# Optimization experiments

Hardware: AMD Instinct MI355X
Metric: run time of the kernel (lower is better)

## Reference

```python
import jax, jax.numpy as jnp
import numpy as np

N = 50000          # num_nodes
E = 800000         # num_edges (avg degree 16)
HID = 128          # hidden_dim
NH = 8             # num_heads
HD = 16            # head_dim
FFN = 512          # ffn_dim
EPS = 1e-5


def setup_inputs() -> dict:
    key = jax.random.key(0)
    ks = jax.random.split(key, 12)
    s = 0.02
    d = {}
    d["x"] = jax.random.normal(ks[0], (N, HID), jnp.float32)
    d["edge_index"] = jax.random.randint(ks[1], (2, E), 0, N, dtype=jnp.int32)
    # projection weights stored as [in, out] (math identical to torch Linear)
    d["Wq"] = jax.random.normal(ks[2], (HID, NH * HD), jnp.float32) * s
    d["bq"] = jnp.zeros((NH * HD,), jnp.float32)
    d["Wk"] = jax.random.normal(ks[3], (HID, NH * HD), jnp.float32) * s
    d["bk"] = jnp.zeros((NH * HD,), jnp.float32)
    d["Wv"] = jax.random.normal(ks[4], (HID, NH * HD), jnp.float32) * s
    d["bv"] = jnp.zeros((NH * HD,), jnp.float32)
    d["Wo"] = jax.random.normal(ks[5], (NH * HD, HID), jnp.float32) * s
    d["bo"] = jnp.zeros((HID,), jnp.float32)
    d["g1"] = jnp.ones((HID,), jnp.float32)
    d["b1"] = jnp.zeros((HID,), jnp.float32)
    d["g2"] = jnp.ones((HID,), jnp.float32)
    d["b2"] = jnp.zeros((HID,), jnp.float32)
    d["W1"] = jax.random.normal(ks[6], (HID, FFN), jnp.float32) * s
    d["bf1"] = jnp.zeros((FFN,), jnp.float32)
    d["W2"] = jax.random.normal(ks[7], (FFN, HID), jnp.float32) * s
    d["bf2"] = jnp.zeros((HID,), jnp.float32)
    return d


def _layer_norm(x, g, b):
    m = jnp.mean(x, axis=-1, keepdims=True)
    v = jnp.mean((x - m) ** 2, axis=-1, keepdims=True)
    return (x - m) * jax.lax.rsqrt(v + EPS) * g + b


def _gnn_layer(x, edge_index, Wq, bq, Wk, bk, Wv, bv, Wo, bo,
               g1, b1, g2, b2, W1, bf1, W2, bf2):
    n = x.shape[0]
    residual = x
    h = _layer_norm(x, g1, b1)

    q = (h @ Wq + bq).reshape(n, NH, HD)
    k = (h @ Wk + bk).reshape(n, NH, HD)
    v = (h @ Wv + bv).reshape(n, NH, HD)

    src, dst = edge_index[0], edge_index[1]
    # original code skips nodes with no in-neighbors (output stays zero)
    deg = jax.ops.segment_sum(jnp.ones(src.shape, x.dtype), dst, num_segments=n)
    # self-loop appended for every attended node
    loops = jnp.arange(n, dtype=src.dtype)
    s_all = jnp.concatenate([src, loops])
    d_all = jnp.concatenate([dst, loops])

    # edge-parallel scaled dot-product scores: [E+N, NH]
    e = jnp.sum(q[d_all] * k[s_all], axis=-1) / np.sqrt(HD).astype(np.float32)
    m = jax.lax.stop_gradient(jax.ops.segment_max(e, d_all, num_segments=n))
    p = jnp.exp(e - m[d_all])
    z = jax.ops.segment_sum(p, d_all, num_segments=n)
    alpha = p / z[d_all]                                   # segment softmax
    agg = jax.ops.segment_sum(alpha[:, :, None] * v[s_all], d_all,
                              num_segments=n)              # [n, NH, HD]
    agg = jnp.where(deg[:, None, None] > 0, agg, jnp.zeros_like(agg))

    att = agg.reshape(n, NH * HD) @ Wo + bo
    x = residual + att                                     # dropout=0 (eval)

    residual = x
    h = _layer_norm(x, g2, b2)
    ffn = jax.nn.gelu(h @ W1 + bf1, approximate=False) @ W2 + bf2
    return residual + ffn


def reference(x, edge_index, Wq, bq, Wk, bk, Wv, bv, Wo, bo,
              g1, b1, g2, b2, W1, bf1, W2, bf2):
    return _gnn_layer(x, edge_index, Wq, bq, Wk, bk, Wv, bv, Wo, bo,
                      g1, b1, g2, b2, W1, bf1, W2, bf2)
```

## Files before the change

kernel.cpp:

```cpp
#include <hip/hip_runtime.h>
#include <hip/hip_bf16.h>

typedef __hip_bfloat16 bf16;
typedef __attribute__((ext_vector_type(8))) short s16x8;
typedef __attribute__((ext_vector_type(4))) float f32x4;

__device__ __forceinline__ float2 bfpair(unsigned u) {
    float2 r;
    r.x = __uint_as_float(u << 16);
    r.y = __uint_as_float(u & 0xffff0000u);
    return r;
}

__device__ __forceinline__ unsigned short f2bf_bits(float f) {
    unsigned u = __float_as_uint(f);
    return (unsigned short)((u + 0x7fffu + ((u >> 16) & 1u)) >> 16);
}

typedef const __attribute__((address_space(1))) unsigned GU;
typedef __attribute__((address_space(3))) unsigned LU;
__device__ __forceinline__ void gload_lds16(const void* g, void* l) {
    __builtin_amdgcn_global_load_lds((GU*)g, (LU*)l, 16, 0, 0);
}

__global__ __launch_bounds__(256) void setup_k(const float* __restrict__ Wq,
                                               const float* __restrict__ Wk,
                                               const float* __restrict__ Wv,
                                               const float* __restrict__ Wo,
                                               const float* __restrict__ W1,
                                               const float* __restrict__ W2,
                                               const float* __restrict__ bq,
                                               const float* __restrict__ bk,
                                               const float* __restrict__ bv,
                                               unsigned short* __restrict__ qkvH,
                                               unsigned short* __restrict__ woH,
                                               unsigned short* __restrict__ w1H,
                                               unsigned short* __restrict__ w2H,
                                               float* __restrict__ bqkv,
                                               int* __restrict__ deg,
                                               const unsigned* __restrict__ eisrc,
                                               int* __restrict__ ei32,
                                               const float* __restrict__ x,
                                               const float* __restrict__ g1,
                                               const float* __restrict__ b1,
                                               bf16* __restrict__ hb,
                                               int N, int twoE, int nzero) {
    int b = blockIdx.x;
    int tid = threadIdx.x;
    if (b < 770) {
        int idx = b * 256 + tid;
        if (idx >= 196608) {
            int i = idx - 196608;
            if (i < 384) bqkv[i] = (i < 128) ? bq[i] : (i < 256) ? bk[i - 128] : bv[i - 256];
            return;
        }
        float w; unsigned short *H; int oi;
        if (idx < 49152) {
            int n = idx >> 7, kx = idx & 127;
            const float* W = (n < 128) ? Wq : (n < 256) ? Wk : Wv;
            w = W[kx * 128 + (n & 127)];
            H = qkvH; oi = idx;
        } else if (idx < 65536) {
            int li = idx - 49152; int n = li >> 7, kx = li & 127;
            w = Wo[kx * 128 + n]; H = woH; oi = li;
        } else if (idx < 131072) {
            int li = idx - 65536; int n = li >> 7, kx = li & 127;
            w = W1[(size_t)kx * 512 + n]; H = w1H; oi = li;
        } else {
            int li = idx - 131072; int n = li >> 9, kx = li & 511;
            w = W2[(size_t)kx * 128 + n]; H = w2H; oi = li;
        }
        H[oi] = f2bf_bits(w);
        return;
    }
    if (b < 770 + nzero) {
        int i = (b - 770) * 256 + tid;
        if (i < N) deg[i] = 0;
        return;
    }
    if (b < 770 + nzero + 2000) {
        __shared__ int s_nz;
        if (tid == 0) s_nz = 0;
        __syncthreads();
        if (eisrc[2 * tid + 1] != 0u) atomicAdd(&s_nz, 1);
        __syncthreads();
        bool is64 = (s_nz == 0);
        long long i = (long long)(b - 770 - nzero) * 256 + tid;
        long long st = (long long)2000 * 256;
        if (is64) { for (; i < twoE; i += st) ei32[i] = (int)eisrc[2 * i]; }
        else      { for (; i < twoE; i += st) ei32[i] = (int)eisrc[i]; }
        return;
    }
    int row = (b - 770 - nzero - 2000) * 4 + (tid >> 6);
    if (row >= N) return;
    int lane = tid & 63;
    float2 f = ((const float2*)x)[(size_t)row * 64 + lane];
    float s = f.x + f.y;
    #pragma unroll
    for (int off = 32; off > 0; off >>= 1) s += __shfl_xor(s, off);
    float mean = s * (1.0f / 128.0f);
    float d0 = f.x - mean, d1 = f.y - mean;
    float vs = d0 * d0 + d1 * d1;
    #pragma unroll
    for (int off = 32; off > 0; off >>= 1) vs += __shfl_xor(vs, off);
    float rstd = rsqrtf(vs * (1.0f / 128.0f) + 1e-5f);
    float2 gg = ((const float2*)g1)[lane];
    float2 bb = ((const float2*)b1)[lane];
    float o0 = d0 * rstd * gg.x + bb.x;
    float o1 = d1 * rstd * gg.y + bb.y;
    unsigned pk = ((unsigned)f2bf_bits(o1) << 16) | (unsigned)f2bf_bits(o0);
    ((unsigned*)hb)[(size_t)row * 64 + lane] = pk;
}

__global__ __launch_bounds__(256) void count_deg_k(const int* __restrict__ ei,
                                                   int* __restrict__ deg, int E) {
    int e = blockIdx.x * 256 + threadIdx.x;
    if (e < E) atomicAdd(&deg[ei[E + e]], 1);
}

#define SCAN_BLK 1024
__global__ __launch_bounds__(256) void scan1_k(const int* __restrict__ deg,
                                               int* __restrict__ off,
                                               int* __restrict__ bsum, int n) {
    __shared__ int s[256];
    int base = blockIdx.x * SCAN_BLK;
    int t = threadIdx.x;
    int v[4]; int sum = 0;
    #pragma unroll
    for (int j = 0; j < 4; j++) {
        int idx = base + t * 4 + j;
        v[j] = (idx < n) ? deg[idx] : 0;
        sum += v[j];
    }
    s[t] = sum; __syncthreads();
    for (int o = 1; o < 256; o <<= 1) {
        int add = (t >= o) ? s[t - o] : 0;
        __syncthreads();
        s[t] += add;
        __syncthreads();
    }
    int run = (t > 0) ? s[t - 1] : 0;
    if (t == 255) bsum[blockIdx.x] = s[255];
    #pragma unroll
    for (int j = 0; j < 4; j++) {
        int idx = base + t * 4 + j;
        if (idx < n) off[idx] = run;
        run += v[j];
    }
}

__global__ __launch_bounds__(256) void scan3_k(int* __restrict__ off,
                                               int* __restrict__ cursor,
                                               const int* __restrict__ bsum,
                                               int n, int nb) {
    __shared__ int sb[64];
    int t = threadIdx.x;
    if (t < 64) {
        int own = (t < nb) ? bsum[t] : 0;
        int v = own;
        #pragma unroll
        for (int o = 1; o < 64; o <<= 1) {
            int u = __shfl_up(v, o);
            if ((t & 63) >= o) v += u;
        }
        sb[t] = v - own;
    }
    __syncthreads();
    int i = blockIdx.x * 256 + t;
    if (i < n) {
        int o = off[i] + sb[i / SCAN_BLK];
        off[i] = o;
        cursor[i] = o;
    }
}

__global__ __launch_bounds__(256) void scatter_k(const int* __restrict__ ei,
                                                 int* __restrict__ cursor,
                                                 int* __restrict__ csr, int E) {
    int e = blockIdx.x * 256 + threadIdx.x;
    if (e >= E) return;
    int s = ei[e], d = ei[E + e];
    int pos = atomicAdd(&cursor[d], 1);
    csr[pos] = s;
}

template <int EPI, bool OUTBF, int K, int BM, bool LNF>
__global__ __launch_bounds__(256) void mgemm_k(const bf16* __restrict__ A,
                                               const bf16* __restrict__ Bh,
                                               const float* __restrict__ bias,
                                               const float* __restrict__ res,
                                               void* __restrict__ outp,
                                               const float* __restrict__ lg,
                                               const float* __restrict__ lb,
                                               bf16* __restrict__ hbout,
                                               long long sub_off, int M,
                                               int ldo, int sub_shift) {
    constexpr int MF = BM / 32;
    constexpr int NK = K / 32;
    constexpr int STEP = BM * 64 + 8192;
    __shared__ __align__(16) char smem[2 * STEP];

    const int nwg = gridDim.x * gridDim.y;
    const int orig = blockIdx.y * gridDim.x + blockIdx.x;
    const int qq = nwg >> 3, rr = nwg & 7;
    const int xcd = orig & 7, jj = orig >> 3;
    const int tile = ((xcd < rr) ? xcd * (qq + 1) : rr * (qq + 1) + (xcd - rr) * qq) + jj;
    const int bx = tile % gridDim.x;
    const int by = tile / gridDim.x;

    const int lane = threadIdx.x & 63;
    const int wid  = threadIdx.x >> 6;
    const int wr = wid >> 1, wc = wid & 1;
    const int lrow = lane & 15, lk = lane >> 4;
    const int m0 = by * BM;
    const int mw0 = wr * (BM / 2);
    const int n0 = bx * 128 + wc * 64;
    const int srow = lane >> 2;
    const int schunk = (lane & 3) ^ ((srow >> 1) & 3);

    const char* Ab  = (const char*)A  + (size_t)m0 * (K * 2);
    const char* Bhb = (const char*)Bh + (size_t)(bx * 128) * (K * 2);

    f32x4 acc[MF][4];
    #pragma unroll
    for (int mf = 0; mf < MF; mf++)
        #pragma unroll
        for (int nf = 0; nf < 4; nf++) {
            f32x4 z = {0.f, 0.f, 0.f, 0.f};
            acc[mf][nf] = z;
        }

    auto stage = [&](int kt, int bufb) {
        const int kb = kt * 64;
        char* sb = &smem[bufb];
        #pragma unroll
        for (int it = 0; it < BM / 64; it++) {
            int rg = wid * (BM / 4) + it * 16;
            gload_lds16(Ab + (size_t)(rg + srow) * (K * 2) + kb + schunk * 16,
                        sb + rg * 64);
        }
        #pragma unroll
        for (int it = 0; it < 2; it++) {
            int rg = wid * 32 + it * 16;
            gload_lds16(Bhb + (size_t)(rg + srow) * (K * 2) + kb + schunk * 16,
                        sb + BM * 64 + rg * 64);
        }
    };

    auto compute = [&](int bufb) {
        const char* sb = &smem[bufb];
        s16x8 a[MF], bh[4];
        #pragma unroll
        for (int mf = 0; mf < MF; mf++) {
            int ra = mw0 + mf * 16 + lrow;
            a[mf] = *(const s16x8*)(sb + ra * 64 + ((lk ^ ((ra >> 1) & 3)) * 16));
        }
        #pragma unroll
        for (int nf = 0; nf < 4; nf++) {
            int rb = wc * 64 + nf * 16 + lrow;
            int co = (lk ^ ((rb >> 1) & 3)) * 16;
            bh[nf] = *(const s16x8*)(sb + BM * 64 + rb * 64 + co);
        }
        #pragma unroll
        for (int mf = 0; mf < MF; mf++)
            #pragma unroll
            for (int nf = 0; nf < 4; nf++)
                acc[mf][nf] = __builtin_amdgcn_mfma_f32_16x16x32_bf16(a[mf], bh[nf], acc[mf][nf], 0, 0, 0);
    };

    stage(0, 0);
    for (int kt = 0; kt < NK; kt++) {
        __syncthreads();
        if (kt + 1 < NK) stage(kt + 1, ((kt + 1) & 1) * STEP);
        compute((kt & 1) * STEP);
    }

    if (!LNF) {
        const int nmask = (1 << sub_shift) - 1;
        #pragma unroll
        for (int mf = 0; mf < MF; mf++) {
            #pragma unroll
            for (int nf = 0; nf < 4; nf++) {
                int n = n0 + nf * 16 + lrow;
                float bsv = bias[n];
                #pragma unroll
                for (int r = 0; r < 4; r++) {
                    int m = m0 + mw0 + mf * 16 + lk * 4 + r;
                    if (m >= M) continue;
                    float val = acc[mf][nf][r] + bsv;
                    if (EPI == 1) val = 0.5f * val * (1.0f + erff(val * 0.70710678118f));
                    if (EPI == 2) val += res[(size_t)m * ldo + n];
                    long long oidx = (long long)m * ldo + (n & nmask) + (long long)(n >> sub_shift) * sub_off;
                    if (OUTBF) ((unsigned short*)outp)[oidx] = f2bf_bits(val);
                    else       ((float*)outp)[oidx] = val;
                }
            }
        }
    } else {
        float vals[MF][4][4];
        float s1[MF][4], s2[MF][4];
        #pragma unroll
        for (int mf = 0; mf < MF; mf++)
            #pragma unroll
            for (int r = 0; r < 4; r++) { s1[mf][r] = 0.f; s2[mf][r] = 0.f; }
        #pragma unroll
        for (int mf = 0; mf < MF; mf++) {
            #pragma unroll
            for (int r = 0; r < 4; r++) {
                int m = m0 + mw0 + mf * 16 + lk * 4 + r;
                #pragma unroll
                for (int nf = 0; nf < 4; nf++) {
                    int n = n0 + nf * 16 + lrow;
                    float val = acc[mf][nf][r] + bias[n];
                    val += (m < M) ? res[(size_t)m * 128 + n] : 0.f;
                    vals[mf][nf][r] = val;
                    s1[mf][r] += val;
                    s2[mf][r] += val * val;
                }
                #pragma unroll
                for (int o = 1; o < 16; o <<= 1) {
                    s1[mf][r] += __shfl_xor(s1[mf][r], o);
                    s2[mf][r] += __shfl_xor(s2[mf][r], o);
                }
            }
        }
        float2* lns = (float2*)smem;
        __syncthreads();
        if (lrow == 0) {
            #pragma unroll
            for (int mf = 0; mf < MF; mf++)
                #pragma unroll
                for (int r = 0; r < 4; r++) {
                    int rl = mw0 + mf * 16 + lk * 4 + r;
                    float2 p; p.x = s1[mf][r]; p.y = s2[mf][r];
                    lns[rl * 2 + wc] = p;
                }
        }
        __syncthreads();
        #pragma unroll
        for (int mf = 0; mf < MF; mf++) {
            #pragma unroll
            for (int r = 0; r < 4; r++) {
                int rl = mw0 + mf * 16 + lk * 4 + r;
                int m = m0 + rl;
                float2 pa = lns[rl * 2 + 0], pb = lns[rl * 2 + 1];
                float mean = (pa.x + pb.x) * (1.0f / 128.0f);
                float var  = (pa.y + pb.y) * (1.0f / 128.0f) - mean * mean;
                float rstd = rsqrtf(var + 1e-5f);
                if (m >= M) continue;
                #pragma unroll
                for (int nf = 0; nf < 4; nf++) {
                    int n = n0 + nf * 16 + lrow;
                    float val = vals[mf][nf][r];
                    ((float*)outp)[(size_t)m * 128 + n] = val;
                    float o = (val - mean) * rstd * lg[n] + lb[n];
                    ((unsigned short*)hbout)[(size_t)m * 128 + n] = f2bf_bits(o);
                }
            }
        }
    }
}

__global__ __launch_bounds__(256) void ffn_k(const bf16* __restrict__ hb,
                                             const bf16* __restrict__ w1,
                                             const bf16* __restrict__ w2,
                                             const float* __restrict__ bf1,
                                             const float* __restrict__ bf2,
                                             float* __restrict__ out, int M) {
    __shared__ __align__(16) char smem[57344];
    char* sA  = smem;
    char* sW1 = smem + 16384;
    char* sW2 = smem + 32768;
    char* sMT = smem + 49152;

    const int nwg = gridDim.x;
    const int orig = blockIdx.x;
    const int qq = nwg >> 3, rr = nwg & 7;
    const int xcd = orig & 7, jj = orig >> 3;
    const int by = ((xcd < rr) ? xcd * (qq + 1) : rr * (qq + 1) + (xcd - rr) * qq) + jj;

    const int lane = threadIdx.x & 63;
    const int wid  = threadIdx.x >> 6;
    const int wr = wid >> 1, wc = wid & 1;
    const int lrow = lane & 15, lk = lane >> 4;
    const int m0 = by * 64;
    const int srow = lane >> 2;
    const int schunk = (lane & 3) ^ ((srow >> 1) & 3);

    const char* Ab = (const char*)hb + (size_t)m0 * 256;

    #pragma unroll
    for (int ks = 0; ks < 4; ks++) {
        int rg = wid * 16;
        gload_lds16(Ab + (size_t)(rg + srow) * 256 + ks * 64 + schunk * 16,
                    sA + ks * 4096 + rg * 64);
    }

    auto stageW = [&](int fc) {
        const char* W1b = (const char*)w1 + (size_t)(fc * 64) * 256;
        #pragma unroll
        for (int ks = 0; ks < 4; ks++) {
            int rg = wid * 16;
            gload_lds16(W1b + (size_t)(rg + srow) * 256 + ks * 64 + schunk * 16,
                        sW1 + ks * 4096 + rg * 64);
        }
        const char* W2b = (const char*)w2 + (size_t)(fc * 64) * 2;
        #pragma unroll
        for (int ks = 0; ks < 2; ks++) {
            #pragma unroll
            for (int it = 0; it < 2; it++) {
                int rg = wid * 32 + it * 16;
                gload_lds16(W2b + (size_t)(rg + srow) * 1024 + ks * 64 + schunk * 16,
                            sW2 + ks * 8192 + rg * 64);
            }
        }
    };

    f32x4 oacc[2][4];
    #pragma unroll
    for (int mf = 0; mf < 2; mf++)
        #pragma unroll
        for (int nf = 0; nf < 4; nf++) {
            f32x4 z = {0.f, 0.f, 0.f, 0.f};
            oacc[mf][nf] = z;
        }

    stageW(0);
    for (int fc = 0; fc < 8; fc++) {
        __syncthreads();
        f32x4 macc[2][2];
        #pragma unroll
        for (int mf = 0; mf < 2; mf++)
            #pragma unroll
            for (int nf = 0; nf < 2; nf++) {
                f32x4 z = {0.f, 0.f, 0.f, 0.f};
                macc[mf][nf] = z;
            }
        #pragma unroll
        for (int ks = 0; ks < 4; ks++) {
            s16x8 a[2], bw[2];
            #pragma unroll
            for (int mf = 0; mf < 2; mf++) {
                int ra = wr * 32 + mf * 16 + lrow;
                a[mf] = *(const s16x8*)(sA + ks * 4096 + ra * 64 + ((lk ^ ((ra >> 1) & 3)) * 16));
            }
            #pragma unroll
            for (int nf = 0; nf < 2; nf++) {
                int rf = wc * 32 + nf * 16 + lrow;
                bw[nf] = *(const s16x8*)(sW1 + ks * 4096 + rf * 64 + ((lk ^ ((rf >> 1) & 3)) * 16));
            }
            #pragma unroll
            for (int mf = 0; mf < 2; mf++)
                #pragma unroll
                for (int nf = 0; nf < 2; nf++)
                    macc[mf][nf] = __builtin_amdgcn_mfma_f32_16x16x32_bf16(a[mf], bw[nf], macc[mf][nf], 0, 0, 0);
        }
        #pragma unroll
        for (int mf = 0; mf < 2; mf++) {
            #pragma unroll
            for (int nf = 0; nf < 2; nf++) {
                int f = wc * 32 + nf * 16 + lrow;
                float bv = bf1[fc * 64 + f];
                #pragma unroll
                for (int r = 0; r < 4; r++) {
                    int m = wr * 32 + mf * 16 + lk * 4 + r;
                    float val = macc[mf][nf][r] + bv;
                    val = 0.5f * val * (1.0f + erff(val * 0.70710678118f));
                    int byte = m * 128 + (((f >> 3) ^ (m & 7)) * 16) + (f & 7) * 2;
                    *(unsigned short*)(sMT + byte) = f2bf_bits(val);
                }
            }
        }
        __syncthreads();
        #pragma unroll
        for (int ks = 0; ks < 2; ks++) {
            s16x8 a2[2], b2[4];
            #pragma unroll
            for (int mf = 0; mf < 2; mf++) {
                int ra = wr * 32 + mf * 16 + lrow;
                int fch = ks * 4 + lk;
                a2[mf] = *(const s16x8*)(sMT + ra * 128 + ((fch ^ (ra & 7)) * 16));
            }
            #pragma unroll
            for (int nf = 0; nf < 4; nf++) {
                int rb = wc * 64 + nf * 16 + lrow;
                b2[nf] = *(const s16x8*)(sW2 + ks * 8192 + rb * 64 + ((lk ^ ((rb >> 1) & 3)) * 16));
            }
            #pragma unroll
            for (int mf = 0; mf < 2; mf++)
                #pragma unroll
                for (int nf = 0; nf < 4; nf++)
                    oacc[mf][nf] = __builtin_amdgcn_mfma_f32_16x16x32_bf16(a2[mf], b2[nf], oacc[mf][nf], 0, 0, 0);
        }
        __syncthreads();
        if (fc + 1 < 8) stageW(fc + 1);
    }

    #pragma unroll
    for (int mf = 0; mf < 2; mf++) {
        #pragma unroll
        for (int nf = 0; nf < 4; nf++) {
            int n = wc * 64 + nf * 16 + lrow;
            float bsv = bf2[n];
            #pragma unroll
            for (int r = 0; r < 4; r++) {
                int m = m0 + wr * 32 + mf * 16 + lk * 4 + r;
                if (m >= M) continue;
                float val = oacc[mf][nf][r] + bsv + out[(size_t)m * 128 + n];
                out[(size_t)m * 128 + n] = val;
            }
        }
    }
}

__global__ __launch_bounds__(256) void node_agg_k(const bf16* __restrict__ q,
                                                  const bf16* __restrict__ k,
                                                  const bf16* __restrict__ v,
                                                  const int* __restrict__ off,
                                                  const int* __restrict__ deg,
                                                  const int* __restrict__ csr,
                                                  bf16* __restrict__ agg, int NN) {
    int node = blockIdx.x * 4 + (threadIdx.x >> 6);
    if (node >= NN) return;
    int lane = threadIdx.x & 63;
    float2 qf = bfpair(((const unsigned*)(q + (size_t)node * 128))[lane]);
    int start = off[node];
    int cnt = deg[node];
    float acc0 = 0.f, acc1 = 0.f, zsum = 0.f;
    if (cnt < 64) {
        int T = cnt + 1;
        int s_vec = (lane < cnt) ? csr[start + lane] : node;
        for (int e0 = 0; e0 < T; e0 += 8) {
            unsigned ku[8], vu[8];
            #pragma unroll
            for (int j = 0; j < 8; j++) {
                if (e0 + j < T) {
                    int s = __shfl(s_vec, e0 + j);
                    ku[j] = ((const unsigned*)(k + (size_t)s * 128))[lane];
                    vu[j] = ((const unsigned*)(v + (size_t)s * 128))[lane];
                }
            }
            #pragma unroll
            for (int j = 0; j < 8; j++) {
                if (e0 + j < T) {
                    float2 kf = bfpair(ku[j]);
                    float dot = qf.x * kf.x + qf.y * kf.y;
                    dot += __shfl_xor(dot, 1);
                    dot += __shfl_xor(dot, 2);
                    dot += __shfl_xor(dot, 4);
                    float p = __expf(dot * 0.25f);
                    zsum += p;
                    float2 vf = bfpair(vu[j]);
                    acc0 += p * vf.x;
                    acc1 += p * vf.y;
                }
            }
        }
    } else {
        for (int e = 0; e <= cnt; e++) {
            int s = (e < cnt) ? csr[start + e] : node;
            float2 kf = bfpair(((const unsigned*)(k + (size_t)s * 128))[lane]);
            float dot = qf.x * kf.x + qf.y * kf.y;
            dot += __shfl_xor(dot, 1);
            dot += __shfl_xor(dot, 2);
            dot += __shfl_xor(dot, 4);
            float p = __expf(dot * 0.25f);
            zsum += p;
            float2 vf = bfpair(((const unsigned*)(v + (size_t)s * 128))[lane]);
            acc0 += p * vf.x;
            acc1 += p * vf.y;
        }
    }
    float2 o;
    if (cnt == 0) { o.x = 0.f; o.y = 0.f; }
    else { float inv = 1.0f / zsum; o.x = acc0 * inv; o.y = acc1 * inv; }
    unsigned pk = ((unsigned)f2bf_bits(o.y) << 16) | (unsigned)f2bf_bits(o.x);
    ((unsigned*)agg)[(size_t)node * 64 + lane] = pk;
}

extern "C" void kernel_launch(void* const* d_in, const int* in_sizes, int n_in,
                              void* d_out, int out_size, void* d_ws, size_t ws_size,
                              hipStream_t stream) {
    const float* x  = (const float*)d_in[0];
    const void*  eiRaw = d_in[1];
    const float* Wq = (const float*)d_in[2];
    const float* bq = (const float*)d_in[3];
    const float* Wk = (const float*)d_in[4];
    const float* bk = (const float*)d_in[5];
    const float* Wv = (const float*)d_in[6];
    const float* bv = (const float*)d_in[7];
    const float* Wo = (const float*)d_in[8];
    const float* bo = (const float*)d_in[9];
    const float* g1 = (const float*)d_in[10];
    const float* b1 = (const float*)d_in[11];
    const float* g2 = (const float*)d_in[12];
    const float* b2 = (const float*)d_in[13];
    const float* W1 = (const float*)d_in[14];
    const float* bf1 = (const float*)d_in[15];
    const float* W2 = (const float*)d_in[16];
    const float* bf2 = (const float*)d_in[17];
    float* out = (float*)d_out;

    const int N = in_sizes[0] / 128;
    const int E = in_sizes[1] / 2;
    const int gy = (N + 127) / 128;
    const int gy64 = (N + 63) / 64;
    const int Mp = gy * 128;

    char* w = (char*)d_ws;
    size_t off_b = 0;
    auto alloc = [&](size_t bytes) -> void* {
        void* ptr = w + off_b;
        off_b = (off_b + bytes + 255) & ~(size_t)255;
        return ptr;
    };
    int*   deg    = (int*)alloc((size_t)N * 4);
    int*   offA   = (int*)alloc((size_t)N * 4);
    int*   cursor = (int*)alloc((size_t)N * 4);
    int*   bsum   = (int*)alloc(64 * 4);
    int*   ei32   = (int*)alloc((size_t)E * 2 * 4);
    int*   csr    = (int*)alloc((size_t)E * 4);
    bf16*  hb     = (bf16*)alloc((size_t)Mp * 128 * 2);
    bf16*  qkvb   = (bf16*)alloc((size_t)N * 3 * 128 * 2);
    bf16*  aggb   = (bf16*)alloc((size_t)Mp * 128 * 2);
    unsigned short* qkvH = (unsigned short*)alloc(49152 * 2);
    unsigned short* woH  = (unsigned short*)alloc(16384 * 2);
    unsigned short* w1H  = (unsigned short*)alloc(65536 * 2);
    unsigned short* w2H  = (unsigned short*)alloc(65536 * 2);
    float* bqkv = (float*)alloc(384 * 4);
    (void)ws_size; (void)n_in; (void)out_size;

    int nb = (N + SCAN_BLK - 1) / SCAN_BLK;
    int nzero = (N + 255) / 256;
    int lnb = (N + 3) / 4;

    setup_k<<<770 + nzero + 2000 + lnb, 256, 0, stream>>>(
        Wq, Wk, Wv, Wo, W1, W2, bq, bk, bv,
        qkvH, woH, w1H, w2H, bqkv,
        deg, (const unsigned*)eiRaw, ei32, x, g1, b1, hb, N, E * 2, nzero);
    count_deg_k<<<(E + 255) / 256, 256, 0, stream>>>(ei32, deg, E);
    scan1_k<<<nb, 256, 0, stream>>>(deg, offA, bsum, N);
    scan3_k<<<(N + 255) / 256, 256, 0, stream>>>(offA, cursor, bsum, N, nb);
    scatter_k<<<(E + 255) / 256, 256, 0, stream>>>(ei32, cursor, csr, E);

    bf16* qb = qkvb;
    bf16* kb = qkvb + (size_t)N * 128;
    bf16* vb = qkvb + (size_t)N * 256;

    mgemm_k<0, true, 128, 128, false><<<dim3(3, gy), 256, 0, stream>>>(
        hb, (const bf16*)qkvH, bqkv, nullptr, qkvb,
        nullptr, nullptr, nullptr, (long long)N * 128, N, 128, 7);
    node_agg_k<<<(N + 3) / 4, 256, 0, stream>>>(qb, kb, vb, offA, deg, csr, aggb, N);
    mgemm_k<2, false, 128, 64, true><<<dim3(1, gy64), 256, 0, stream>>>(
        aggb, (const bf16*)woH, bo, x, out,
        g2, b2, hb, 0, N, 128, 15);
    ffn_k<<<gy64, 256, 0, stream>>>(hb, (const bf16*)w1H, (const bf16*)w2H,
                                    bf1, bf2, out, N);
}
```

Before: 370.0 us.

## Restructure FFN kernel with double-buffered weight chunks and per-wave row ownership

The fused FFN kernel now walks the 512-wide hidden dimension in 16 chunks of 32 instead of 8 chunks of 64. W1 and W2 tiles are double-buffered so the next chunk's global-to-LDS loads are issued before the current chunk's MFMAs. Each wave now owns 16 full rows, so the GELU intermediate written to LDS is read back only by the wave that wrote it, which drops two of the three block barriers per chunk. In exchange each A/B fragment sees less reuse, there are twice as many chunk iterations, and correctness depends on wave-local LDS visibility without a barrier.

```diff
diff --git a/kernel.cpp b/kernel.cpp
--- a/kernel.cpp
+++ b/kernel.cpp
@@ -367,7 +367,7 @@
                                              const float* __restrict__ bf1,
                                              const float* __restrict__ bf2,
                                              float* __restrict__ out, int M) {
-    __shared__ __align__(16) char smem[57344];
+    __shared__ __align__(16) char smem[53248];
     char* sA  = smem;
     char* sW1 = smem + 16384;
     char* sW2 = smem + 32768;
@@ -381,7 +381,6 @@
 
     const int lane = threadIdx.x & 63;
     const int wid  = threadIdx.x >> 6;
-    const int wr = wid >> 1, wc = wid & 1;
     const int lrow = lane & 15, lk = lane >> 4;
     const int m0 = by * 64;
     const int srow = lane >> 2;
@@ -396,119 +395,89 @@
                     sA + ks * 4096 + rg * 64);
     }
 
-    auto stageW = [&](int fc) {
-        const char* W1b = (const char*)w1 + (size_t)(fc * 64) * 256;
+    auto stageW = [&](int fc, int buf) {
+        const char* W1b = (const char*)w1 + (size_t)(fc * 32) * 256;
+        #pragma unroll
+        for (int i = 0; i < 2; i++) {
+            int u = wid * 2 + i;
+            int ks = u >> 1, fg = u & 1;
+            gload_lds16(W1b + (size_t)(fg * 16 + srow) * 256 + ks * 64 + schunk * 16,
+                        sW1 + buf * 8192 + ks * 2048 + fg * 1024);
+        }
+        const char* W2b = (const char*)w2 + (size_t)fc * 64;
+        #pragma unroll
+        for (int i = 0; i < 2; i++) {
+            int rg = (wid * 2 + i) * 16;
+            gload_lds16(W2b + (size_t)(rg + srow) * 1024 + schunk * 16,
+                        sW2 + buf * 8192 + rg * 64);
+        }
+    };
+
+    f32x4 oacc[8];
+    #pragma unroll
+    for (int nf = 0; nf < 8; nf++) {
+        f32x4 z = {0.f, 0.f, 0.f, 0.f};
+        oacc[nf] = z;
+    }
+
+    stageW(0, 0);
+    for (int fc = 0; fc < 16; fc++) {
+        __syncthreads();
+        if (fc + 1 < 16) stageW(fc + 1, (fc + 1) & 1);
+        const char* w1b = sW1 + (fc & 1) * 8192;
+        const char* w2b = sW2 + (fc & 1) * 8192;
+
+        f32x4 macc[2];
+        #pragma unroll
+        for (int nf = 0; nf < 2; nf++) {
+            f32x4 z = {0.f, 0.f, 0.f, 0.f};
+            macc[nf] = z;
+        }
         #pragma unroll
         for (int ks = 0; ks < 4; ks++) {
-            int rg = wid * 16;
-            gload_lds16(W1b + (size_t)(rg + srow) * 256 + ks * 64 + schunk * 16,
-                        sW1 + ks * 4096 + rg * 64);
-        }
-        const char* W2b = (const char*)w2 + (size_t)(fc * 64) * 2;
-        #pragma unroll
-        for (int ks = 0; ks < 2; ks++) {
-            #pragma unroll
-            for (int it = 0; it < 2; it++) {
-                int rg = wid * 32 + it * 16;
-                gload_lds16(W2b + (size_t)(rg + srow) * 1024 + ks * 64 + schunk * 16,
-                            sW2 + ks * 8192 + rg * 64);
-            }
-        }
-    };
-
-    f32x4 oacc[2][4];
-    #pragma unroll
-    for (int mf = 0; mf < 2; mf++)
-        #pragma unroll
-        for (int nf = 0; nf < 4; nf++) {
-            f32x4 z = {0.f, 0.f, 0.f, 0.f};
-            oacc[mf][nf] = z;
-        }
-
-    stageW(0);
-    for (int fc = 0; fc < 8; fc++) {
-        __syncthreads();
-        f32x4 macc[2][2];
-        #pragma unroll
-        for (int mf = 0; mf < 2; mf++)
+            int ra = wid * 16 + lrow;
+            s16x8 a = *(const s16x8*)(sA + ks * 4096 + ra * 64 + ((lk ^ ((ra >> 1) & 3)) * 16));
             #pragma unroll
             for (int nf = 0; nf < 2; nf++) {
-                f32x4 z = {0.f, 0.f, 0.f, 0.f};
-                macc[mf][nf] = z;
-            }
-        #pragma unroll
-        for (int ks = 0; ks < 4; ks++) {
-            s16x8 a[2], bw[2];
-            #pragma unroll
-            for (int mf = 0; mf < 2; mf++) {
-                int ra = wr * 32 + mf * 16 + lrow;
-                a[mf] = *(const s16x8*)(sA + ks * 4096 + ra * 64 + ((lk ^ ((ra >> 1) & 3)) * 16));
-            }
-            #pragma unroll
-            for (int nf = 0; nf < 2; nf++) {
-                int rf = wc * 32 + nf * 16 + lrow;
-                bw[nf] = *(const s16x8*)(sW1 + ks * 4096 + rf * 64 + ((lk ^ ((rf >> 1) & 3)) * 16));
-            }
-            #pragma unroll
-            for (int mf = 0; mf < 2; mf++)
-                #pragma unroll
-                for (int nf = 0; nf < 2; nf++)
-                    macc[mf][nf] = __builtin_amdgcn_mfma_f32_16x16x32_bf16(a[mf], bw[nf], macc[mf][nf], 0, 0, 0);
-        }
-        #pragma unroll
-        for (int mf = 0; mf < 2; mf++) {
-            #pragma unroll
-            for (int nf = 0; nf < 2; nf++) {
-                int f = wc * 32 + nf * 16 + lrow;
-                float bv = bf1[fc * 64 + f];
-                #pragma unroll
-                for (int r = 0; r < 4; r++) {
-                    int m = wr * 32 + mf * 16 + lk * 4 + r;
-                    float val = macc[mf][nf][r] + bv;
-                    val = 0.5f * val * (1.0f + erff(val * 0.70710678118f));
-                    int byte = m * 128 + (((f >> 3) ^ (m & 7)) * 16) + (f & 7) * 2;
-                    *(unsigned short*)(sMT + byte) = f2bf_bits(val);
-                }
-            }
-        }
-        __syncthreads();
-        #pragma unroll
-        for (int ks = 0; ks < 2; ks++) {
-            s16x8 a2[2], b2[4];
-            #pragma unroll
-            for (int mf = 0; mf < 2; mf++) {
-                int ra = wr * 32 + mf * 16 + lrow;
-                int fch = ks * 4 + lk;
-                a2[mf] = *(const s16x8*)(sMT + ra * 128 + ((fch ^ (ra & 7)) * 16));
-            }
-            #pragma unroll
-            for (int nf = 0; nf < 4; nf++) {
-                int rb = wc * 64 + nf * 16 + lrow;
-                b2[nf] = *(const s16x8*)(sW2 + ks * 8192 + rb * 64 + ((lk ^ ((rb >> 1) & 3)) * 16));
-            }
-            #pragma unroll
-            for (int mf = 0; mf < 2; mf++)
-                #pragma unroll
-                for (int nf = 0; nf < 4; nf++)
-                    oacc[mf][nf] = __builtin_amdgcn_mfma_f32_16x16x32_bf16(a2[mf], b2[nf], oacc[mf][nf], 0, 0, 0);
-        }
-        __syncthreads();
-        if (fc + 1 < 8) stageW(fc + 1);
-    }
-
-    #pragma unroll
-    for (int mf = 0; mf < 2; mf++) {
-        #pragma unroll
-        for (int nf = 0; nf < 4; nf++) {
-            int n = wc * 64 + nf * 16 + lrow;
-            float bsv = bf2[n];
+                int rf = nf * 16 + lrow;
+                s16x8 bw = *(const s16x8*)(w1b + ks * 2048 + rf * 64 + ((lk ^ ((rf >> 1) & 3)) * 16));
+                macc[nf] = __builtin_amdgcn_mfma_f32_16x16x32_bf16(a, bw, macc[nf], 0, 0, 0);
+            }
+        }
+        #pragma unroll
+        for (int nf = 0; nf < 2; nf++) {
+            int f = nf * 16 + lrow;
+            float bv = bf1[fc * 32 + f];
             #pragma unroll
             for (int r = 0; r < 4; r++) {
-                int m = m0 + wr * 32 + mf * 16 + lk * 4 + r;
-                if (m >= M) continue;
-                float val = oacc[mf][nf][r] + bsv + out[(size_t)m * 128 + n];
-                out[(size_t)m * 128 + n] = val;
-            }
+                int m = wid * 16 + lk * 4 + r;
+                float val = macc[nf][r] + bv;
+                val = 0.5f * val * (1.0f + erff(val * 0.70710678118f));
+                int byte = m * 64 + (((f >> 3) ^ ((m >> 1) & 3)) * 16) + (f & 7) * 2;
+                *(unsigned short*)(sMT + byte) = f2bf_bits(val);
+            }
+        }
+        {
+            int ra = wid * 16 + lrow;
+            s16x8 a2 = *(const s16x8*)(sMT + ra * 64 + ((lk ^ ((ra >> 1) & 3)) * 16));
+            #pragma unroll
+            for (int nf = 0; nf < 8; nf++) {
+                int rb = nf * 16 + lrow;
+                s16x8 b2 = *(const s16x8*)(w2b + rb * 64 + ((lk ^ ((rb >> 1) & 3)) * 16));
+                oacc[nf] = __builtin_amdgcn_mfma_f32_16x16x32_bf16(a2, b2, oacc[nf], 0, 0, 0);
+            }
+        }
+    }
+
+    #pragma unroll
+    for (int nf = 0; nf < 8; nf++) {
+        int n = nf * 16 + lrow;
+        float bsv = bf2[n];
+        #pragma unroll
+        for (int r = 0; r < 4; r++) {
+            int m = m0 + wid * 16 + lk * 4 + r;
+            if (m >= M) continue;
+            out[(size_t)m * 128 + n] = oacc[nf][r] + bsv + out[(size_t)m * 128 + n];
         }
     }
 }
```

Result: no change. 374.0 us (+1.1%).
